# Optimization experiments

Hardware: AMD Instinct MI355X
Metric: run time of the kernel (lower is better)

Reference implementation:

```python
import jax, jax.numpy as jnp
import numpy as np

M, K, D = 64, 32, 32   # antennas, users, hidden features
PT = 1.0               # total transmit power
BS = 1024


def _glorot(key, shape):
    fan_out, fan_in = shape
    lim = np.sqrt(6.0 / (fan_in + fan_out)).astype(np.float32)
    return jax.random.uniform(key, shape, minval=-lim, maxval=lim, dtype=jnp.float32)


def setup_inputs() -> dict:
    key = jax.random.key(0)
    ks = jax.random.split(key, 16)
    inp = {"x": jax.random.normal(ks[0], (BS, M, K, 2), dtype=jnp.float32)}
    dims = [(D, 2), (D, D), (D, D), (D, D), (2, D)]
    i = 1
    for l, sh in enumerate(dims, start=1):
        for tag in ("s", "m", "k"):
            inp[f"W{l}{tag}"] = _glorot(ks[i], sh)
            i += 1
    return inp


def gnn_layer(x, Ws, Wm, Wk):
    # x: (b, M, K, d_in); weights: (d_out, d_in)
    msg_m = jnp.sum(x, axis=2)  # (b, M, d_in) aggregate over users per antenna
    msg_k = jnp.sum(x, axis=1)  # (b, K, d_in) aggregate over antennas per user
    z = (jnp.einsum('hd,bmkd->bmkh', Ws, x)
         + jnp.einsum('hd,bmd->bmh', Wm, msg_m)[:, :, None, :]
         + jnp.einsum('hd,bkd->bkh', Wk, msg_k)[:, None, :, :])
    return z  # (b, M, K, d_out)


def pwr_norm(x):
    # x: (b, M, K, 2) -> |W|_F^2 = sum over m,k of re^2+im^2
    power = jnp.sum(x * x, axis=(1, 2, 3), keepdims=True)
    alpha = jnp.sqrt(PT / power)
    return alpha * x


def reference(x, W1s, W1m, W1k, W2s, W2m, W2k, W3s, W3m, W3k,
              W4s, W4m, W4k, W5s, W5m, W5k):
    h = jax.nn.relu(gnn_layer(x, W1s, W1m, W1k))
    h = jax.nn.relu(gnn_layer(h, W2s, W2m, W2k))
    h = jax.nn.relu(gnn_layer(h, W3s, W3m, W3k))
    h = jax.nn.relu(gnn_layer(h, W4s, W4m, W4k))
    h = gnn_layer(h, W5s, W5m, W5k)
    return pwr_norm(h)
```

## Files before the change

kernel.cpp:

```cpp
#include <hip/hip_runtime.h>
#include <hip/hip_fp16.h>


namespace {

constexpr int NTHREADS = 1024;
constexpr float INPUT_SCALE = 0.0625f;
constexpr float LAYER_SCALE = 0.0078125f;

typedef _Float16 half8 __attribute__((ext_vector_type(8)));
typedef float    f32x4 __attribute__((ext_vector_type(4)));
typedef unsigned uint4v __attribute__((ext_vector_type(4)));

#define RPT32(X) X(0)X(1)X(2)X(3)X(4)X(5)X(6)X(7)X(8)X(9)X(10)X(11)X(12)X(13)X(14)X(15) \
                 X(16)X(17)X(18)X(19)X(20)X(21)X(22)X(23)X(24)X(25)X(26)X(27)X(28)X(29)X(30)X(31)
#define RPT16P(X) X(0,0,1)X(1,2,3)X(2,4,5)X(3,6,7)X(4,8,9)X(5,10,11)X(6,12,13)X(7,14,15) \
                  X(8,16,17)X(9,18,19)X(10,20,21)X(11,22,23)X(12,24,25)X(13,26,27)X(14,28,29)X(15,30,31)

__device__ __forceinline__ unsigned pk(float a, float b) {
    __half2 h = __floats2half2_rn(a, b);
    return *reinterpret_cast<unsigned*>(&h);
}
__device__ __forceinline__ float2 upk(unsigned w) {
    __half2 h;
    *reinterpret_cast<unsigned*>(&h) = w;
    return __half22float2(h);
}

__device__ __forceinline__ half8 load_xfrag(const unsigned* base18, int row, int quad) {
    const unsigned* ap = base18 + row * 18 + quad * 4;
    const uint2 p0 = *reinterpret_cast<const uint2*>(ap);
    const uint2 p1 = *reinterpret_cast<const uint2*>(ap + 2);
    uint4v raw;
    raw.x = p0.x; raw.y = p0.y; raw.z = p1.x; raw.w = p1.y;
    return __builtin_bit_cast(half8, raw);
}

__device__ __forceinline__ half8 load_wfrag(const float* __restrict__ W, int h, int quad) {
    const float4* wr = reinterpret_cast<const float4*>(W + h * 32 + quad * 8);
    const float4 w0 = wr[0];
    const float4 w1 = wr[1];
    half8 b;
    b[0] = (_Float16)w0.x; b[1] = (_Float16)w0.y; b[2] = (_Float16)w0.z; b[3] = (_Float16)w0.w;
    b[4] = (_Float16)w1.x; b[5] = (_Float16)w1.y; b[6] = (_Float16)w1.z; b[7] = (_Float16)w1.w;
    return b;
}

__device__ __forceinline__ void phase_msg(const unsigned* __restrict__ Xh,
                                          unsigned* __restrict__ MSG, int t) {
    if (t >= 512) {
        const int item = t - 512;
        const int fp2 = item & 7, m = item >> 3;
        float s0 = 0.f, s1 = 0.f, s2 = 0.f, s3 = 0.f;
#pragma unroll 8
        for (int kk = 0; kk < 32; ++kk) {
            const int k = (kk + 3 * m) & 31;
            const uint2 u = *reinterpret_cast<const uint2*>(Xh + (m * 32 + k) * 18 + fp2 * 2);
            const float2 p = upk(u.x), q = upk(u.y);
            s0 += p.x; s1 += p.y; s2 += q.x; s3 += q.y;
        }
        uint2 r; r.x = pk(s0, s1); r.y = pk(s2, s3);
        *reinterpret_cast<uint2*>(MSG + m * 18 + fp2 * 2) = r;
    } else if (t < 256) {
        const int k = t >> 3, fp2 = t & 7;
        float s0 = 0.f, s1 = 0.f, s2 = 0.f, s3 = 0.f;
#pragma unroll 8
        for (int mm = 0; mm < 64; ++mm) {
            const uint2 u = *reinterpret_cast<const uint2*>(Xh + (mm * 32 + k) * 18 + fp2 * 2);
            const float2 p = upk(u.x), q = upk(u.y);
            s0 += p.x; s1 += p.y; s2 += q.x; s3 += q.y;
        }
        uint2 r; r.x = pk(s0, s1); r.y = pk(s2, s3);
        *reinterpret_cast<uint2*>(MSG + (64 + k) * 18 + fp2 * 2) = r;
    }
}

__device__ __forceinline__ void phase_small(const float* __restrict__ Wmg,
                                            const float* __restrict__ Wkg,
                                            const unsigned* __restrict__ MSG,
                                            unsigned* __restrict__ ABu, int t) {
    const int w = t >> 6, lane = t & 63;
    if (w < 12) {
        const int isb = (w >= 8);
        const int ww = isb ? (w - 8) : w;
        const int mt = ww >> 1, nt = ww & 1;
        const int rowbase = (isb ? 64 : 0) + mt * 16;
        const int quad = lane >> 4, col = lane & 15;
        const half8 a = load_xfrag(MSG, rowbase + col, quad);
        const int h = nt * 16 + col;
        const half8 b = load_wfrag(isb ? Wkg : Wmg, h, quad);
        f32x4 c = {0.f, 0.f, 0.f, 0.f};
        c = __builtin_amdgcn_mfma_f32_16x16x32_f16(a, b, c, 0, 0, 0);
        _Float16* ABf = reinterpret_cast<_Float16*>(ABu);
        const int r0 = rowbase + quad * 4;
        ABf[(r0 + 0) * 36 + h] = (_Float16)c[0];
        ABf[(r0 + 1) * 36 + h] = (_Float16)c[1];
        ABf[(r0 + 2) * 36 + h] = (_Float16)c[2];
        ABf[(r0 + 3) * 36 + h] = (_Float16)c[3];
    }
}

__device__ __forceinline__ void phase_main(const float* __restrict__ Wsg,
                                           unsigned* __restrict__ Xh,
                                           const unsigned* __restrict__ ABu, int t) {
    const int w = t >> 6, lane = t & 63;
    const int quad = lane >> 4, col = lane & 15;
    const half8 a0 = load_wfrag(Wsg, col, quad);
    const half8 a1 = load_wfrag(Wsg, 16 + col, quad);
    const uint2* AB2 = reinterpret_cast<const uint2*>(ABu);
#pragma unroll 2
    for (int i = 0; i < 8; ++i) {
        const int T = w + i * 16;
        const int node0 = T * 16;
        const int m = T >> 1;
        const int k0 = (T & 1) * 16;
        const half8 b = load_xfrag(Xh, node0 + col, quad);
        const int krow = 64 + k0 + col;
        const uint2 Am0 = AB2[m * 9 + quad];
        const uint2 Am1 = AB2[m * 9 + 4 + quad];
        const uint2 Bk0 = AB2[krow * 9 + quad];
        const uint2 Bk1 = AB2[krow * 9 + 4 + quad];
        const float2 a0p = upk(Am0.x), a0q = upk(Am0.y);
        const float2 a1p = upk(Am1.x), a1q = upk(Am1.y);
        const float2 b0p = upk(Bk0.x), b0q = upk(Bk0.y);
        const float2 b1p = upk(Bk1.x), b1q = upk(Bk1.y);
        f32x4 c0, c1;
        c0[0] = a0p.x + b0p.x; c0[1] = a0p.y + b0p.y;
        c0[2] = a0q.x + b0q.x; c0[3] = a0q.y + b0q.y;
        c1[0] = a1p.x + b1p.x; c1[1] = a1p.y + b1p.y;
        c1[2] = a1q.x + b1q.x; c1[3] = a1q.y + b1q.y;
        c0 = __builtin_amdgcn_mfma_f32_16x16x32_f16(a0, b, c0, 0, 0, 0);
        c1 = __builtin_amdgcn_mfma_f32_16x16x32_f16(a1, b, c1, 0, 0, 0);
        uint2 w0, w1;
        w0.x = pk(fmaxf(c0[0], 0.f) * LAYER_SCALE, fmaxf(c0[1], 0.f) * LAYER_SCALE);
        w0.y = pk(fmaxf(c0[2], 0.f) * LAYER_SCALE, fmaxf(c0[3], 0.f) * LAYER_SCALE);
        w1.x = pk(fmaxf(c1[0], 0.f) * LAYER_SCALE, fmaxf(c1[1], 0.f) * LAYER_SCALE);
        w1.y = pk(fmaxf(c1[2], 0.f) * LAYER_SCALE, fmaxf(c1[3], 0.f) * LAYER_SCALE);
        unsigned* dst = Xh + (node0 + col) * 18 + quad * 2;
        *reinterpret_cast<uint2*>(dst) = w0;
        *reinterpret_cast<uint2*>(dst + 8) = w1;
    }
}

__global__ void __launch_bounds__(NTHREADS) gnn_fused(
    const float* __restrict__ xg,
    const float* __restrict__ w1s, const float* __restrict__ w1m, const float* __restrict__ w1k,
    const float* __restrict__ w2s, const float* __restrict__ w2m, const float* __restrict__ w2k,
    const float* __restrict__ w3s, const float* __restrict__ w3m, const float* __restrict__ w3k,
    const float* __restrict__ w4s, const float* __restrict__ w4m, const float* __restrict__ w4k,
    const float* __restrict__ w5s, const float* __restrict__ w5m, const float* __restrict__ w5k,
    float* __restrict__ out)
{
    __shared__ __align__(16) unsigned Xh[2048 * 18];
    __shared__ __align__(16) unsigned MSG[96 * 18];
    __shared__ __align__(16) unsigned ABu[96 * 18];
    __shared__ float red[17];

    const int t = threadIdx.x;
    const int b = blockIdx.x;
    const int k = t & 31;
    const int m1 = t >> 5;
    const int m2 = m1 + 32;
    const int lane = t & 63;
    const int wave = t >> 6;

    float2 a1 = *reinterpret_cast<const float2*>(xg + (size_t)b * 4096 + 2 * t);
    float2 a2 = *reinterpret_cast<const float2*>(xg + (size_t)b * 4096 + 2048 + 2 * t);
    a1.x *= INPUT_SCALE; a1.y *= INPUT_SCALE;
    a2.x *= INPUT_SCALE; a2.y *= INPUT_SCALE;

    _Float16* ABf = reinterpret_cast<_Float16*>(ABu);
    float* MSGf = reinterpret_cast<float*>(MSG);

    if (t < 64) MSGf[t] = 0.f;
    __syncthreads();
    {
        float s0 = a1.x + a2.x, s1 = a1.y + a2.y;
        s0 += __shfl_xor(s0, 32);
        s1 += __shfl_xor(s1, 32);
        if (lane < 32) {
            atomicAdd(&MSGf[2 * k], s0);
            atomicAdd(&MSGf[2 * k + 1], s1);
        }
        float f0 = a1.x, f1 = a1.y, g0 = a2.x, g1 = a2.y;
#pragma unroll
        for (int mask = 1; mask <= 16; mask <<= 1) {
            f0 += __shfl_xor(f0, mask); f1 += __shfl_xor(f1, mask);
            g0 += __shfl_xor(g0, mask); g1 += __shfl_xor(g1, mask);
        }
        const float2 wm = *reinterpret_cast<const float2*>(w1m + 2 * k);
        ABf[m1 * 36 + k] = (_Float16)(wm.x * f0 + wm.y * f1);
        ABf[m2 * 36 + k] = (_Float16)(wm.x * g0 + wm.y * g1);
    }
    __syncthreads();
    {
        const int kk = t >> 5, hh = t & 31;
        const float2 wk2 = *reinterpret_cast<const float2*>(w1k + 2 * hh);
        ABf[(64 + kk) * 36 + hh] = (_Float16)(wk2.x * MSGf[2 * kk] + wk2.y * MSGf[2 * kk + 1]);
    }
    __syncthreads();
#pragma unroll 1
    for (int half = 0; half < 2; ++half) {
        const int n = half ? (t + 1024) : t;
        const int m = half ? m2 : m1;
        const float xa = half ? a2.x : a1.x;
        const float xb = half ? a2.y : a1.y;
#define DECL_ACC(h) float acc##h = (float)ABf[m * 36 + h] + (float)ABf[(64 + k) * 36 + h] \
                                 + w1s[h * 2] * xa + w1s[h * 2 + 1] * xb;
        RPT32(DECL_ACC)
#undef DECL_ACC
#define ST(p, h0, h1) Xh[n * 18 + p] = pk(fmaxf(acc##h0, 0.f) * LAYER_SCALE, \
                                          fmaxf(acc##h1, 0.f) * LAYER_SCALE);
        RPT16P(ST)
#undef ST
    }
    __syncthreads();

    phase_msg(Xh, MSG, t); __syncthreads();
    phase_small(w2m, w2k, MSG, ABu, t); __syncthreads();
    phase_main(w2s, Xh, ABu, t); __syncthreads();

    phase_msg(Xh, MSG, t); __syncthreads();
    phase_small(w3m, w3k, MSG, ABu, t); __syncthreads();
    phase_main(w3s, Xh, ABu, t); __syncthreads();

    phase_msg(Xh, MSG, t); __syncthreads();
    phase_small(w4m, w4k, MSG, ABu, t); __syncthreads();
    phase_main(w4s, Xh, ABu, t); __syncthreads();

    phase_msg(Xh, MSG, t); __syncthreads();
    if (t < 128) {
        const int m = t & 63, h = t >> 6;
        float acc = 0.f;
#pragma unroll
        for (int p = 0; p < 16; ++p) {
            const float2 u = upk(MSG[m * 18 + p]);
            acc += w5m[h * 32 + 2 * p] * u.x + w5m[h * 32 + 2 * p + 1] * u.y;
        }
        ABf[m * 36 + h] = (_Float16)acc;
    } else if (t < 192) {
        const int idx = t - 128;
        const int kk = idx & 31, h = idx >> 5;
        float acc = 0.f;
#pragma unroll
        for (int p = 0; p < 16; ++p) {
            const float2 u = upk(MSG[(64 + kk) * 18 + p]);
            acc += w5k[h * 32 + 2 * p] * u.x + w5k[h * 32 + 2 * p + 1] * u.y;
        }
        ABf[(64 + kk) * 36 + h] = (_Float16)acc;
    }
    __syncthreads();

    float za0 = (float)ABf[m1 * 36 + 0] + (float)ABf[(64 + k) * 36 + 0];
    float za1 = (float)ABf[m1 * 36 + 1] + (float)ABf[(64 + k) * 36 + 1];
    float zb0 = (float)ABf[m2 * 36 + 0] + (float)ABf[(64 + k) * 36 + 0];
    float zb1 = (float)ABf[m2 * 36 + 1] + (float)ABf[(64 + k) * 36 + 1];
#pragma unroll
    for (int p = 0; p < 16; ++p) {
        const float2 u = upk(Xh[t * 18 + p]);
        za0 += w5s[2 * p] * u.x + w5s[2 * p + 1] * u.y;
        za1 += w5s[32 + 2 * p] * u.x + w5s[32 + 2 * p + 1] * u.y;
        const float2 v = upk(Xh[(t + 1024) * 18 + p]);
        zb0 += w5s[2 * p] * v.x + w5s[2 * p + 1] * v.y;
        zb1 += w5s[32 + 2 * p] * v.x + w5s[32 + 2 * p + 1] * v.y;
    }

    float p2 = za0 * za0 + za1 * za1 + zb0 * zb0 + zb1 * zb1;
#pragma unroll
    for (int mask = 1; mask <= 32; mask <<= 1) p2 += __shfl_xor(p2, mask);
    if (lane == 0) red[wave] = p2;
    __syncthreads();
    if (t == 0) {
        float tot = 0.f;
#pragma unroll
        for (int i = 0; i < 16; ++i) tot += red[i];
        red[16] = rsqrtf(tot);
    }
    __syncthreads();
    const float alpha = red[16];

    float2 r1, r2;
    r1.x = alpha * za0; r1.y = alpha * za1;
    r2.x = alpha * zb0; r2.y = alpha * zb1;
    *reinterpret_cast<float2*>(out + (size_t)b * 4096 + 2 * t) = r1;
    *reinterpret_cast<float2*>(out + (size_t)b * 4096 + 2048 + 2 * t) = r2;
}

}

extern "C" void kernel_launch(void* const* d_in, const int* in_sizes, int n_in,
                              void* d_out, int out_size, void* d_ws, size_t ws_size,
                              hipStream_t stream) {
    const float* xg  = (const float*)d_in[0];
    const float* w1s = (const float*)d_in[1];
    const float* w1m = (const float*)d_in[2];
    const float* w1k = (const float*)d_in[3];
    const float* w2s = (const float*)d_in[4];
    const float* w2m = (const float*)d_in[5];
    const float* w2k = (const float*)d_in[6];
    const float* w3s = (const float*)d_in[7];
    const float* w3m = (const float*)d_in[8];
    const float* w3k = (const float*)d_in[9];
    const float* w4s = (const float*)d_in[10];
    const float* w4m = (const float*)d_in[11];
    const float* w4k = (const float*)d_in[12];
    const float* w5s = (const float*)d_in[13];
    const float* w5m = (const float*)d_in[14];
    const float* w5k = (const float*)d_in[15];
    float* out = (float*)d_out;

    hipLaunchKernelGGL(gnn_fused, dim3(1024), dim3(NTHREADS), 0, stream,
                       xg, w1s, w1m, w1k, w2s, w2m, w2k, w3s, w3m, w3k,
                       w4s, w4m, w4k, w5s, w5m, w5k, out);
}
```

Before: 222.0 us.

## Split activations into two feature planes and use packed fp16 math with DPP reductions

```diff
diff --git a/kernel.cpp b/kernel.cpp
--- a/kernel.cpp
+++ b/kernel.cpp
@@ -7,8 +7,10 @@
 constexpr int NTHREADS = 1024;
 constexpr float INPUT_SCALE = 0.0625f;
 constexpr float LAYER_SCALE = 0.0078125f;
+constexpr int XPLANE = 16384;
 
 typedef _Float16 half8 __attribute__((ext_vector_type(8)));
+typedef _Float16 half2v __attribute__((ext_vector_type(2)));
 typedef float    f32x4 __attribute__((ext_vector_type(4)));
 typedef unsigned uint4v __attribute__((ext_vector_type(4)));
 
@@ -17,61 +19,79 @@
 #define RPT16P(X) X(0,0,1)X(1,2,3)X(2,4,5)X(3,6,7)X(4,8,9)X(5,10,11)X(6,12,13)X(7,14,15) \
                   X(8,16,17)X(9,18,19)X(10,20,21)X(11,22,23)X(12,24,25)X(13,26,27)X(14,28,29)X(15,30,31)
 
-__device__ __forceinline__ unsigned pk(float a, float b) {
-    __half2 h = __floats2half2_rn(a, b);
-    return *reinterpret_cast<unsigned*>(&h);
-}
+#define AB_OFF(h) ((((h) >> 2) & 3) * 8 + (((h) >> 4) & 1) * 4 + ((h) & 3))
+
 __device__ __forceinline__ float2 upk(unsigned w) {
     __half2 h;
     *reinterpret_cast<unsigned*>(&h) = w;
     return __half22float2(h);
 }
-
-__device__ __forceinline__ half8 load_xfrag(const unsigned* base18, int row, int quad) {
-    const unsigned* ap = base18 + row * 18 + quad * 4;
-    const uint2 p0 = *reinterpret_cast<const uint2*>(ap);
-    const uint2 p1 = *reinterpret_cast<const uint2*>(ap + 2);
-    uint4v raw;
-    raw.x = p0.x; raw.y = p0.y; raw.z = p1.x; raw.w = p1.y;
-    return __builtin_bit_cast(half8, raw);
-}
-
-__device__ __forceinline__ half8 load_wfrag(const float* __restrict__ W, int h, int quad) {
+__device__ __forceinline__ unsigned pkz(float a, float b) {
+    auto h = __builtin_amdgcn_cvt_pkrtz(a, b);
+    return __builtin_bit_cast(unsigned, h);
+}
+__device__ __forceinline__ unsigned hadd2u(unsigned a, unsigned b) {
+    half2v x = __builtin_bit_cast(half2v, a);
+    half2v y = __builtin_bit_cast(half2v, b);
+    return __builtin_bit_cast(unsigned, x + y);
+}
+__device__ __forceinline__ unsigned hmax0u(unsigned a) {
+    unsigned r;
+    asm("v_pk_max_f16 %0, %1, 0" : "=v"(r) : "v"(a));
+    return r;
+}
+template <int CTRL>
+__device__ __forceinline__ uint4v dpp_hadd(uint4v s) {
+    uint4v r;
+    r.x = hadd2u(s.x, (unsigned)__builtin_amdgcn_mov_dpp((int)s.x, CTRL, 0xF, 0xF, true));
+    r.y = hadd2u(s.y, (unsigned)__builtin_amdgcn_mov_dpp((int)s.y, CTRL, 0xF, 0xF, true));
+    r.z = hadd2u(s.z, (unsigned)__builtin_amdgcn_mov_dpp((int)s.z, CTRL, 0xF, 0xF, true));
+    r.w = hadd2u(s.w, (unsigned)__builtin_amdgcn_mov_dpp((int)s.w, CTRL, 0xF, 0xF, true));
+    return r;
+}
+
+__device__ __forceinline__ half8 load_wfrag(const float* __restrict__ W, int h, int quad,
+                                            float scale) {
     const float4* wr = reinterpret_cast<const float4*>(W + h * 32 + quad * 8);
     const float4 w0 = wr[0];
     const float4 w1 = wr[1];
     half8 b;
-    b[0] = (_Float16)w0.x; b[1] = (_Float16)w0.y; b[2] = (_Float16)w0.z; b[3] = (_Float16)w0.w;
-    b[4] = (_Float16)w1.x; b[5] = (_Float16)w1.y; b[6] = (_Float16)w1.z; b[7] = (_Float16)w1.w;
+    b[0] = (_Float16)(w0.x * scale); b[1] = (_Float16)(w0.y * scale);
+    b[2] = (_Float16)(w0.z * scale); b[3] = (_Float16)(w0.w * scale);
+    b[4] = (_Float16)(w1.x * scale); b[5] = (_Float16)(w1.y * scale);
+    b[6] = (_Float16)(w1.z * scale); b[7] = (_Float16)(w1.w * scale);
     return b;
 }
 
-__device__ __forceinline__ void phase_msg(const unsigned* __restrict__ Xh,
+__device__ __forceinline__ void phase_msg(const unsigned* __restrict__ Xs,
                                           unsigned* __restrict__ MSG, int t) {
-    if (t >= 512) {
-        const int item = t - 512;
-        const int fp2 = item & 7, m = item >> 3;
-        float s0 = 0.f, s1 = 0.f, s2 = 0.f, s3 = 0.f;
-#pragma unroll 8
-        for (int kk = 0; kk < 32; ++kk) {
-            const int k = (kk + 3 * m) & 31;
-            const uint2 u = *reinterpret_cast<const uint2*>(Xh + (m * 32 + k) * 18 + fp2 * 2);
-            const float2 p = upk(u.x), q = upk(u.y);
-            s0 += p.x; s1 += p.y; s2 += q.x; s3 += q.y;
-        }
-        uint2 r; r.x = pk(s0, s1); r.y = pk(s2, s3);
-        *reinterpret_cast<uint2*>(MSG + m * 18 + fp2 * 2) = r;
-    } else if (t < 256) {
-        const int k = t >> 3, fp2 = t & 7;
-        float s0 = 0.f, s1 = 0.f, s2 = 0.f, s3 = 0.f;
-#pragma unroll 8
-        for (int mm = 0; mm < 64; ++mm) {
-            const uint2 u = *reinterpret_cast<const uint2*>(Xh + (mm * 32 + k) * 18 + fp2 * 2);
-            const float2 p = upk(u.x), q = upk(u.y);
-            s0 += p.x; s1 += p.y; s2 += q.x; s3 += q.y;
-        }
-        uint2 r; r.x = pk(s0, s1); r.y = pk(s2, s3);
-        *reinterpret_cast<uint2*>(MSG + (64 + k) * 18 + fp2 * 2) = r;
+    if (t < 512) {
+        const int k = t >> 4, fq = (t >> 2) & 3, mq = t & 3;
+        const unsigned* p = Xs + (fq >> 1) * XPLANE + mq * 4096 + k * 8 + (fq & 1) * 4;
+        half8 accA{}, accB{};
+#pragma unroll
+        for (int i = 0; i < 16; i += 2) {
+            accA += __builtin_bit_cast(half8, *(const uint4v*)(p + i * 256));
+            accB += __builtin_bit_cast(half8, *(const uint4v*)(p + (i + 1) * 256));
+        }
+        uint4v s = __builtin_bit_cast(uint4v, accA + accB);
+        s = dpp_hadd<0xB1>(s);
+        s = dpp_hadd<0x4E>(s);
+        if (mq == 0) *(uint4v*)(MSG + (64 + k) * 20 + fq * 4) = s;
+    } else {
+        const int u = t - 512;
+        const int m = u >> 3, fq = (u >> 1) & 3, kh = u & 1;
+        const unsigned* base = Xs + (fq >> 1) * XPLANE + m * 256 + kh * 128 + (fq & 1) * 4;
+        const unsigned rot = (unsigned)((m & 15) * 8);
+        half8 accA{}, accB{};
+#pragma unroll
+        for (int i = 0; i < 16; i += 2) {
+            accA += __builtin_bit_cast(half8, *(const uint4v*)(base + (((unsigned)(i * 8)) ^ rot)));
+            accB += __builtin_bit_cast(half8, *(const uint4v*)(base + (((unsigned)((i + 1) * 8)) ^ rot)));
+        }
+        uint4v s = __builtin_bit_cast(uint4v, accA + accB);
+        s = dpp_hadd<0xB1>(s);
+        if (kh == 0) *(uint4v*)(MSG + m * 20 + fq * 4) = s;
     }
 }
 
@@ -83,62 +103,56 @@
     if (w < 12) {
         const int isb = (w >= 8);
         const int ww = isb ? (w - 8) : w;
-        const int mt = ww >> 1, nt = ww & 1;
-        const int rowbase = (isb ? 64 : 0) + mt * 16;
+        const int nt = ww >> 1, ht = ww & 1;
         const int quad = lane >> 4, col = lane & 15;
-        const half8 a = load_xfrag(MSG, rowbase + col, quad);
-        const int h = nt * 16 + col;
-        const half8 b = load_wfrag(isb ? Wkg : Wmg, h, quad);
+        const int rowbase = (isb ? 64 : 0) + nt * 16;
+        const uint4v mraw = *(const uint4v*)(MSG + (rowbase + col) * 20 + quad * 4);
+        const half8 bfrag = __builtin_bit_cast(half8, mraw);
+        const half8 afrag = load_wfrag(isb ? Wkg : Wmg, ht * 16 + col, quad, LAYER_SCALE);
         f32x4 c = {0.f, 0.f, 0.f, 0.f};
-        c = __builtin_amdgcn_mfma_f32_16x16x32_f16(a, b, c, 0, 0, 0);
-        _Float16* ABf = reinterpret_cast<_Float16*>(ABu);
-        const int r0 = rowbase + quad * 4;
-        ABf[(r0 + 0) * 36 + h] = (_Float16)c[0];
-        ABf[(r0 + 1) * 36 + h] = (_Float16)c[1];
-        ABf[(r0 + 2) * 36 + h] = (_Float16)c[2];
-        ABf[(r0 + 3) * 36 + h] = (_Float16)c[3];
+        c = __builtin_amdgcn_mfma_f32_16x16x32_f16(afrag, bfrag, c, 0, 0, 0);
+        uint2 st;
+        st.x = pkz(c[0], c[1]);
+        st.y = pkz(c[2], c[3]);
+        *reinterpret_cast<uint2*>(ABu + (rowbase + col) * 20 + quad * 4 + ht * 2) = st;
     }
 }
 
 __device__ __forceinline__ void phase_main(const float* __restrict__ Wsg,
-                                           unsigned* __restrict__ Xh,
+                                           unsigned* __restrict__ Xs,
                                            const unsigned* __restrict__ ABu, int t) {
     const int w = t >> 6, lane = t & 63;
     const int quad = lane >> 4, col = lane & 15;
-    const half8 a0 = load_wfrag(Wsg, col, quad);
-    const half8 a1 = load_wfrag(Wsg, 16 + col, quad);
-    const uint2* AB2 = reinterpret_cast<const uint2*>(ABu);
+    const half8 a0 = load_wfrag(Wsg, col, quad, LAYER_SCALE);
+    const half8 a1 = load_wfrag(Wsg, 16 + col, quad, LAYER_SCALE);
+    const uint4v* AB4 = reinterpret_cast<const uint4v*>(ABu);
+    const unsigned* xr = Xs + (quad >> 1) * XPLANE + col * 8 + (quad & 1) * 4;
+    unsigned* xw = Xs + col * 8 + quad * 2;
 #pragma unroll 2
     for (int i = 0; i < 8; ++i) {
         const int T = w + i * 16;
         const int node0 = T * 16;
         const int m = T >> 1;
         const int k0 = (T & 1) * 16;
-        const half8 b = load_xfrag(Xh, node0 + col, quad);
+        const half8 b = __builtin_bit_cast(half8, *(const uint4v*)(xr + node0 * 8));
         const int krow = 64 + k0 + col;
-        const uint2 Am0 = AB2[m * 9 + quad];
-        const uint2 Am1 = AB2[m * 9 + 4 + quad];
-        const uint2 Bk0 = AB2[krow * 9 + quad];
-        const uint2 Bk1 = AB2[krow * 9 + 4 + quad];
-        const float2 a0p = upk(Am0.x), a0q = upk(Am0.y);
-        const float2 a1p = upk(Am1.x), a1q = upk(Am1.y);
-        const float2 b0p = upk(Bk0.x), b0q = upk(Bk0.y);
-        const float2 b1p = upk(Bk1.x), b1q = upk(Bk1.y);
-        f32x4 c0, c1;
-        c0[0] = a0p.x + b0p.x; c0[1] = a0p.y + b0p.y;
-        c0[2] = a0q.x + b0q.x; c0[3] = a0q.y + b0q.y;
-        c1[0] = a1p.x + b1p.x; c1[1] = a1p.y + b1p.y;
-        c1[2] = a1q.x + b1q.x; c1[3] = a1q.y + b1q.y;
+        const uint4v Am = AB4[m * 5 + quad];
+        const uint4v Bk = AB4[krow * 5 + quad];
+        const float2 p00 = upk(hadd2u(Am.x, Bk.x));
+        const float2 p01 = upk(hadd2u(Am.y, Bk.y));
+        const float2 p10 = upk(hadd2u(Am.z, Bk.z));
+        const float2 p11 = upk(hadd2u(Am.w, Bk.w));
+        f32x4 c0 = {p00.x, p00.y, p01.x, p01.y};
+        f32x4 c1 = {p10.x, p10.y, p11.x, p11.y};
         c0 = __builtin_amdgcn_mfma_f32_16x16x32_f16(a0, b, c0, 0, 0, 0);
         c1 = __builtin_amdgcn_mfma_f32_16x16x32_f16(a1, b, c1, 0, 0, 0);
         uint2 w0, w1;
-        w0.x = pk(fmaxf(c0[0], 0.f) * LAYER_SCALE, fmaxf(c0[1], 0.f) * LAYER_SCALE);
-        w0.y = pk(fmaxf(c0[2], 0.f) * LAYER_SCALE, fmaxf(c0[3], 0.f) * LAYER_SCALE);
-        w1.x = pk(fmaxf(c1[0], 0.f) * LAYER_SCALE, fmaxf(c1[1], 0.f) * LAYER_SCALE);
-        w1.y = pk(fmaxf(c1[2], 0.f) * LAYER_SCALE, fmaxf(c1[3], 0.f) * LAYER_SCALE);
-        unsigned* dst = Xh + (node0 + col) * 18 + quad * 2;
-        *reinterpret_cast<uint2*>(dst) = w0;
-        *reinterpret_cast<uint2*>(dst + 8) = w1;
+        w0.x = hmax0u(pkz(c0[0], c0[1]));
+        w0.y = hmax0u(pkz(c0[2], c0[3]));
+        w1.x = hmax0u(pkz(c1[0], c1[1]));
+        w1.y = hmax0u(pkz(c1[2], c1[3]));
+        *reinterpret_cast<uint2*>(xw + node0 * 8) = w0;
+        *reinterpret_cast<uint2*>(xw + node0 * 8 + XPLANE) = w1;
     }
 }
 
@@ -151,9 +165,9 @@
     const float* __restrict__ w5s, const float* __restrict__ w5m, const float* __restrict__ w5k,
     float* __restrict__ out)
 {
-    __shared__ __align__(16) unsigned Xh[2048 * 18];
-    __shared__ __align__(16) unsigned MSG[96 * 18];
-    __shared__ __align__(16) unsigned ABu[96 * 18];
+    __shared__ __align__(16) unsigned Xs[2 * XPLANE];
+    __shared__ __align__(16) unsigned MSG[96 * 20];
+    __shared__ __align__(16) unsigned ABu[96 * 20];
     __shared__ float red[17];
 
     const int t = threadIdx.x;
@@ -189,80 +203,99 @@
             g0 += __shfl_xor(g0, mask); g1 += __shfl_xor(g1, mask);
         }
         const float2 wm = *reinterpret_cast<const float2*>(w1m + 2 * k);
-        ABf[m1 * 36 + k] = (_Float16)(wm.x * f0 + wm.y * f1);
-        ABf[m2 * 36 + k] = (_Float16)(wm.x * g0 + wm.y * g1);
+        ABf[m1 * 40 + AB_OFF(k)] = (_Float16)(wm.x * f0 + wm.y * f1);
+        ABf[m2 * 40 + AB_OFF(k)] = (_Float16)(wm.x * g0 + wm.y * g1);
     }
     __syncthreads();
     {
         const int kk = t >> 5, hh = t & 31;
         const float2 wk2 = *reinterpret_cast<const float2*>(w1k + 2 * hh);
-        ABf[(64 + kk) * 36 + hh] = (_Float16)(wk2.x * MSGf[2 * kk] + wk2.y * MSGf[2 * kk + 1]);
+        ABf[(64 + kk) * 40 + AB_OFF(hh)] =
+            (_Float16)(wk2.x * MSGf[2 * kk] + wk2.y * MSGf[2 * kk + 1]);
     }
     __syncthreads();
 #pragma unroll 1
-    for (int half = 0; half < 2; ++half) {
-        const int n = half ? (t + 1024) : t;
-        const int m = half ? m2 : m1;
-        const float xa = half ? a2.x : a1.x;
-        const float xb = half ? a2.y : a1.y;
-#define DECL_ACC(h) float acc##h = (float)ABf[m * 36 + h] + (float)ABf[(64 + k) * 36 + h] \
+    for (int hf = 0; hf < 2; ++hf) {
+        const int n = hf ? (t + 1024) : t;
+        const int m = hf ? m2 : m1;
+        const float xa = hf ? a2.x : a1.x;
+        const float xb = hf ? a2.y : a1.y;
+#define DECL_ACC(h) float acc##h = (float)ABf[m * 40 + AB_OFF(h)] \
+                                 + (float)ABf[(64 + k) * 40 + AB_OFF(h)] \
                                  + w1s[h * 2] * xa + w1s[h * 2 + 1] * xb;
         RPT32(DECL_ACC)
 #undef DECL_ACC
-#define ST(p, h0, h1) Xh[n * 18 + p] = pk(fmaxf(acc##h0, 0.f) * LAYER_SCALE, \
-                                          fmaxf(acc##h1, 0.f) * LAYER_SCALE);
+        unsigned tmp[16];
+#define ST(p, h0, h1) tmp[p] = pkz(fmaxf(acc##h0, 0.f) * LAYER_SCALE, \
+                                   fmaxf(acc##h1, 0.f) * LAYER_SCALE);
         RPT16P(ST)
 #undef ST
-    }
-    __syncthreads();
-
-    phase_msg(Xh, MSG, t); __syncthreads();
+        unsigned* xd = Xs + n * 8;
+        uint4v v0, v1, v2, v3;
+        v0.x = tmp[0];  v0.y = tmp[1];  v0.z = tmp[2];  v0.w = tmp[3];
+        v1.x = tmp[4];  v1.y = tmp[5];  v1.z = tmp[6];  v1.w = tmp[7];
+        v2.x = tmp[8];  v2.y = tmp[9];  v2.z = tmp[10]; v2.w = tmp[11];
+        v3.x = tmp[12]; v3.y = tmp[13]; v3.z = tmp[14]; v3.w = tmp[15];
+        *reinterpret_cast<uint4v*>(xd) = v0;
+        *reinterpret_cast<uint4v*>(xd + 4) = v1;
+        *reinterpret_cast<uint4v*>(xd + XPLANE) = v2;
+        *reinterpret_cast<uint4v*>(xd + XPLANE + 4) = v3;
+    }
+    __syncthreads();
+
+    phase_msg(Xs, MSG, t); __syncthreads();
     phase_small(w2m, w2k, MSG, ABu, t); __syncthreads();
-    phase_main(w2s, Xh, ABu, t); __syncthreads();
-
-    phase_msg(Xh, MSG, t); __syncthreads();
+    phase_main(w2s, Xs, ABu, t); __syncthreads();
+
+    phase_msg(Xs, MSG, t); __syncthreads();
     phase_small(w3m, w3k, MSG, ABu, t); __syncthreads();
-    phase_main(w3s, Xh, ABu, t); __syncthreads();
-
-    phase_msg(Xh, MSG, t); __syncthreads();
+    phase_main(w3s, Xs, ABu, t); __syncthreads();
+
+    phase_msg(Xs, MSG, t); __syncthreads();
     phase_small(w4m, w4k, MSG, ABu, t); __syncthreads();
-    phase_main(w4s, Xh, ABu, t); __syncthreads();
-
-    phase_msg(Xh, MSG, t); __syncthreads();
+    phase_main(w4s, Xs, ABu, t); __syncthreads();
+
+    phase_msg(Xs, MSG, t); __syncthreads();
     if (t < 128) {
         const int m = t & 63, h = t >> 6;
         float acc = 0.f;
 #pragma unroll
         for (int p = 0; p < 16; ++p) {
-            const float2 u = upk(MSG[m * 18 + p]);
+            const float2 u = upk(MSG[m * 20 + p]);
             acc += w5m[h * 32 + 2 * p] * u.x + w5m[h * 32 + 2 * p + 1] * u.y;
         }
-        ABf[m * 36 + h] = (_Float16)acc;
+        ABf[m * 40 + h] = (_Float16)acc;
     } else if (t < 192) {
         const int idx = t - 128;
         const int kk = idx & 31, h = idx >> 5;
         float acc = 0.f;
 #pragma unroll
         for (int p = 0; p < 16; ++p) {
-            const float2 u = upk(MSG[(64 + kk) * 18 + p]);
+            const float2 u = upk(MSG[(64 + kk) * 20 + p]);
             acc += w5k[h * 32 + 2 * p] * u.x + w5k[h * 32 + 2 * p + 1] * u.y;
         }
-        ABf[(64 + kk) * 36 + h] = (_Float16)acc;
-    }
-    __syncthreads();
-
-    float za0 = (float)ABf[m1 * 36 + 0] + (float)ABf[(64 + k) * 36 + 0];
-    float za1 = (float)ABf[m1 * 36 + 1] + (float)ABf[(64 + k) * 36 + 1];
-    float zb0 = (float)ABf[m2 * 36 + 0] + (float)ABf[(64 + k) * 36 + 0];
-    float zb1 = (float)ABf[m2 * 36 + 1] + (float)ABf[(64 + k) * 36 + 1];
-#pragma unroll
-    for (int p = 0; p < 16; ++p) {
-        const float2 u = upk(Xh[t * 18 + p]);
-        za0 += w5s[2 * p] * u.x + w5s[2 * p + 1] * u.y;
-        za1 += w5s[32 + 2 * p] * u.x + w5s[32 + 2 * p + 1] * u.y;
-        const float2 v = upk(Xh[(t + 1024) * 18 + p]);
-        zb0 += w5s[2 * p] * v.x + w5s[2 * p + 1] * v.y;
-        zb1 += w5s[32 + 2 * p] * v.x + w5s[32 + 2 * p + 1] * v.y;
+        ABf[(64 + kk) * 40 + h] = (_Float16)acc;
+    }
+    __syncthreads();
+
+    float za0 = (float)ABf[m1 * 40 + 0] + (float)ABf[(64 + k) * 40 + 0];
+    float za1 = (float)ABf[m1 * 40 + 1] + (float)ABf[(64 + k) * 40 + 1];
+    float zb0 = (float)ABf[m2 * 40 + 0] + (float)ABf[(64 + k) * 40 + 0];
+    float zb1 = (float)ABf[m2 * 40 + 1] + (float)ABf[(64 + k) * 40 + 1];
+    {
+        const unsigned* xa0 = Xs + t * 8;
+        const unsigned* xb0 = Xs + (t + 1024) * 8;
+#pragma unroll
+        for (int p = 0; p < 16; ++p) {
+            const unsigned ua = (p < 8) ? xa0[p] : xa0[XPLANE + (p - 8)];
+            const float2 u = upk(ua);
+            za0 += w5s[2 * p] * u.x + w5s[2 * p + 1] * u.y;
+            za1 += w5s[32 + 2 * p] * u.x + w5s[32 + 2 * p + 1] * u.y;
+            const unsigned ub = (p < 8) ? xb0[p] : xb0[XPLANE + (p - 8)];
+            const float2 v = upk(ub);
+            zb0 += w5s[2 * p] * v.x + w5s[2 * p + 1] * v.y;
+            zb1 += w5s[32 + 2 * p] * v.x + w5s[32 + 2 * p + 1] * v.y;
+        }
     }
 
     float p2 = za0 * za0 + za1 * za1 + zb0 * zb0 + zb1 * zb1;
```

Result: faster. 209.5 us (-5.6%).
